# Kernel tuning notes

Hardware: AMD Instinct MI355X
Metric: run time of the kernel (lower is better)

Reference implementation:

```python
import jax, jax.numpy as jnp
import numpy as np

B, S, D = 32, 1024, 256
K, H, L = 64, 4, 4
KH, DV = K // H, D // H  # pooling key size per head, pooling value size
EPS = 1e-5
SCALE = 1.0 / np.sqrt(K).astype(np.float32)  # both encoder and pooling use sqrt(1/key_size)


def _ln(x, gamma=None, beta=None):
    m = jnp.mean(x, axis=-1, keepdims=True)
    v = jnp.mean(jnp.square(x - m), axis=-1, keepdims=True)
    y = (x - m) * jax.lax.rsqrt(v + EPS)
    if gamma is not None:
        y = y * gamma + beta
    return y


def setup_inputs() -> dict:
    key = jax.random.key(0)
    ks = iter(jax.random.split(key, 32))

    def w(shape, fan_in):
        return jax.random.normal(next(ks), shape, jnp.float32) / np.sqrt(fan_in).astype(np.float32)

    inp = {
        "input": jax.random.normal(next(ks), (B, S, D), jnp.float32),
        "lin0_W": w((D, D), D), "lin0_b": jnp.zeros((D,), jnp.float32),
        # stacked params for the 4 AttentionEncoder layers
        "enc_Wk": w((L, D, K), D), "enc_bk": jnp.zeros((L, K), jnp.float32),
        "enc_Wq": w((L, D, K), D), "enc_bq": jnp.zeros((L, K), jnp.float32),
        "enc_Wv": w((L, D, D), D), "enc_bv": jnp.zeros((L, D), jnp.float32),
        "enc_Wb": w((L, D, 1), D), "enc_bb": jnp.zeros((L, 1), jnp.float32),
        "enc_Wff": w((L, D, D), D), "enc_bff": jnp.zeros((L, D), jnp.float32),
        "enc_g1": jnp.ones((L, D), jnp.float32), "enc_beta1": jnp.zeros((L, D), jnp.float32),
        # multi-head pooling head
        "pool_Wk": w((D, KH), D), "pool_bk": jnp.zeros((KH,), jnp.float32),
        "pool_Wv": w((D, DV), D), "pool_bv": jnp.zeros((DV,), jnp.float32),
        "queries": jax.random.normal(next(ks), (H, KH), jnp.float32),
        "lin1_W": w((D, 2), D), "lin1_b": jnp.zeros((2,), jnp.float32),
    }
    return inp


def reference(input, lin0_W, lin0_b, enc_Wk, enc_bk, enc_Wq, enc_bq, enc_Wv, enc_bv,
              enc_Wb, enc_bb, enc_Wff, enc_bff, enc_g1, enc_beta1,
              pool_Wk, pool_bk, pool_Wv, pool_bv, queries, lin1_W, lin1_b):
    # NOTE: original code computes act0(lin0(input)) and then discards it (dead code);
    # it is omitted here since it does not affect the output.
    x = input
    for i in range(L):
        k = (x @ enc_Wk[i] + enc_bk[i]) * SCALE          # [B,S,K]
        q = x @ enc_Wq[i] + enc_bq[i]                     # [B,S,K]
        v = x @ enc_Wv[i] + enc_bv[i]                     # [B,S,D]
        bias = x @ enc_Wb[i] + enc_bb[i]                  # [B,S,1], broadcast over columns
        scores = jax.nn.sigmoid(jnp.einsum('bik,bjk->bij', k, q) + bias)  # [B,S,S]
        attn = jnp.einsum('bij,bjd->bid', scores, v)      # [B,S,D]
        res = _ln(x + attn, enc_g1[i], enc_beta1[i])
        ff = jax.nn.relu(res @ enc_Wff[i] + enc_bff[i])
        x = _ln(res + ff)                                 # norm2: no affine
    # multi-head pooling with learned queries
    pk = (x @ pool_Wk + pool_bk) * SCALE                  # [B,S,KH]
    pv = x @ pool_Wv + pool_bv                            # [B,S,DV]
    sc = jnp.einsum('bsk,hk->bsh', pk, queries)           # [B,S,H]
    sc = jax.nn.softmax(sc, axis=1)                       # softmax over sequence
    pooled = jnp.einsum('bsh,bsd->bhd', sc, pv).reshape(x.shape[0], -1)  # [B, H*DV]=[B,D]
    return pooled @ lin1_W + lin1_b                       # [B,2]
```

## Files before the change

kernel.cpp:

```cpp
#include <hip/hip_runtime.h>
#include <hip/hip_bf16.h>
#include <math.h>

#define BB 32
#define SS 1024
#define DD 256
#define MM (BB*SS)
#define LEPS 1e-5f

typedef __bf16 bf16x8 __attribute__((ext_vector_type(8)));
typedef __bf16 bf16x4 __attribute__((ext_vector_type(4)));
typedef float f32x4 __attribute__((ext_vector_type(4)));

__global__ __launch_bounds__(256) void cast_wt(const float* __restrict__ W,
                                               __bf16* __restrict__ WT,
                                               int N, float scale, int dstride, int noff) {
    int n = blockIdx.x, l = blockIdx.z, k = threadIdx.x;
    WT[(size_t)dstride * l + (size_t)(n + noff) * 256 + k] =
        (__bf16)(W[(size_t)256 * N * l + (size_t)k * N + n] * scale);
}

__global__ __launch_bounds__(128) void bias_combine(const float* __restrict__ bk,
                                                    const float* __restrict__ bq,
                                                    float* __restrict__ dst) {
    int l = blockIdx.x, j = threadIdx.x;
    dst[l * 128 + j] = (j < 64) ? bk[l * 64 + j] * 0.125f : bq[l * 64 + (j - 64)];
}

__global__ __launch_bounds__(256) void cast_x(const float* __restrict__ x, __bf16* __restrict__ xb) {
    size_t i = ((size_t)blockIdx.x * 256 + threadIdx.x) * 8;
    float4 a = *(const float4*)(x + i);
    float4 b = *(const float4*)(x + i + 4);
    __bf16 o[8] __attribute__((aligned(16)));
    o[0] = (__bf16)a.x; o[1] = (__bf16)a.y; o[2] = (__bf16)a.z; o[3] = (__bf16)a.w;
    o[4] = (__bf16)b.x; o[5] = (__bf16)b.y; o[6] = (__bf16)b.z; o[7] = (__bf16)b.w;
    *(bf16x8*)(xb + i) = *(bf16x8*)o;
}

template <int BN, int MODE>
__global__ __launch_bounds__(256) void gemm_mfma(const __bf16* __restrict__ A,
                                                 const __bf16* __restrict__ WT,
                                                 const float* __restrict__ bias,
                                                 float bscale, int relu,
                                                 void* __restrict__ Cv, void* __restrict__ Cv2,
                                                 int N) {
    constexpr int MR = (BN == 128) ? 4 : 2;
    constexpr int NC = (BN == 128) ? 4 : BN / 16;
    const int t = threadIdx.x;
    const int w = t >> 6, lane = t & 63;
    const int m0 = blockIdx.x * 128;
    const int n0 = blockIdx.y * BN;
    const size_t wt_z = (MODE == 3) ? (size_t)blockIdx.z * SS * 256 : 0;
    const size_t c_z  = (MODE == 3) ? (size_t)blockIdx.z * 256 * (size_t)N : 0;
    const int wr = (BN == 128) ? (w >> 1) * 64 : w * 32;
    const int wc = (BN == 128) ? (w & 1) * 64 : 0;
    __shared__ __align__(16) __bf16 Al[128][64];
    __shared__ __align__(16) __bf16 Wl[BN][64];
    f32x4 acc[MR][NC] = {};

    for (int k0 = 0; k0 < 256; k0 += 64) {
        __syncthreads();
        {
            int r = t >> 1, half = t & 1;
            const __bf16* src = A + (size_t)(m0 + r) * 256 + k0 + half * 32;
            bf16x8 v0 = *(const bf16x8*)(src);
            bf16x8 v1 = *(const bf16x8*)(src + 8);
            bf16x8 v2 = *(const bf16x8*)(src + 16);
            bf16x8 v3 = *(const bf16x8*)(src + 24);
            int cb = half * 4;
            *(bf16x8*)&Al[r][((cb + 0) ^ (r & 7)) * 8] = v0;
            *(bf16x8*)&Al[r][((cb + 1) ^ (r & 7)) * 8] = v1;
            *(bf16x8*)&Al[r][((cb + 2) ^ (r & 7)) * 8] = v2;
            *(bf16x8*)&Al[r][((cb + 3) ^ (r & 7)) * 8] = v3;
        }
        if (BN == 128) {
            int r = t >> 1, half = t & 1;
            const __bf16* src = WT + wt_z + (size_t)(n0 + r) * 256 + k0 + half * 32;
            bf16x8 v0 = *(const bf16x8*)(src);
            bf16x8 v1 = *(const bf16x8*)(src + 8);
            bf16x8 v2 = *(const bf16x8*)(src + 16);
            bf16x8 v3 = *(const bf16x8*)(src + 24);
            int cb = half * 4;
            *(bf16x8*)&Wl[r][((cb + 0) ^ (r & 7)) * 8] = v0;
            *(bf16x8*)&Wl[r][((cb + 1) ^ (r & 7)) * 8] = v1;
            *(bf16x8*)&Wl[r][((cb + 2) ^ (r & 7)) * 8] = v2;
            *(bf16x8*)&Wl[r][((cb + 3) ^ (r & 7)) * 8] = v3;
        } else if (BN == 64) {
            int n = t >> 2, q = t & 3;
            const __bf16* src = WT + (size_t)(n0 + n) * 256 + k0 + q * 16;
            bf16x8 v0 = *(const bf16x8*)src;
            bf16x8 v1 = *(const bf16x8*)(src + 8);
            *(bf16x8*)&Wl[n][((q * 2 + 0) ^ (n & 7)) * 8] = v0;
            *(bf16x8*)&Wl[n][((q * 2 + 1) ^ (n & 7)) * 8] = v1;
        } else {
            if (t < 128) {
                int n = t >> 3, c = t & 7;
                bf16x8 v = *(const bf16x8*)(WT + (size_t)(n0 + n) * 256 + k0 + c * 8);
                *(bf16x8*)&Wl[n][(c ^ (n & 7)) * 8] = v;
            }
        }
        __syncthreads();
#pragma unroll
        for (int ks = 0; ks < 2; ks++) {
            int c = ks * 4 + (lane >> 4);
            bf16x8 af[MR];
#pragma unroll
            for (int mf = 0; mf < MR; mf++) {
                int i = wr + mf * 16 + (lane & 15);
                af[mf] = *(const bf16x8*)&Al[i][(c ^ (i & 7)) * 8];
            }
#pragma unroll
            for (int nf = 0; nf < NC; nf++) {
                int n = wc + nf * 16 + (lane & 15);
                bf16x8 bfr = *(const bf16x8*)&Wl[n][(c ^ (n & 7)) * 8];
#pragma unroll
                for (int mf = 0; mf < MR; mf++)
                    acc[mf][nf] = __builtin_amdgcn_mfma_f32_16x16x32_bf16(af[mf], bfr, acc[mf][nf], 0, 0, 0);
            }
        }
    }
#pragma unroll
    for (int mf = 0; mf < MR; mf++) {
#pragma unroll
        for (int nf = 0; nf < NC; nf++) {
            int col = n0 + wc + nf * 16 + (lane & 15);
            float bcol = (MODE == 3) ? 0.f : bias[col] * bscale;
#pragma unroll
            for (int r = 0; r < 4; r++) {
                int row = m0 + wr + mf * 16 + (lane >> 4) * 4 + r;
                float v = acc[mf][nf][r] + ((MODE == 3) ? bias[row] : bcol);
                if (relu) v = fmaxf(v, 0.f);
                if (MODE == 2) {
                    if (col < 64) ((__bf16*)Cv)[(size_t)row * 64 + col] = (__bf16)v;
                    else ((__bf16*)Cv2)[(size_t)row * 64 + (col - 64)] = (__bf16)v;
                } else if (MODE == 1 || MODE == 3) {
                    ((__bf16*)Cv)[c_z + (size_t)row * N + col] = (__bf16)v;
                } else {
                    ((float*)Cv)[(size_t)row * N + col] = v;
                }
            }
        }
    }
}

__global__ __launch_bounds__(256) void bias_gemv(const float* __restrict__ X,
                                                 const float* __restrict__ Wb,
                                                 const float* __restrict__ bb,
                                                 float* __restrict__ out) {
    int wave = threadIdx.x >> 6, lane = threadIdx.x & 63;
    size_t row = (size_t)blockIdx.x * 4 + wave;
    float4 xv = *(const float4*)(X + row * 256 + lane * 4);
    float4 wv = *(const float4*)(Wb + lane * 4);
    float p = xv.x * wv.x + xv.y * wv.y + xv.z * wv.z + xv.w * wv.w;
    for (int off = 32; off; off >>= 1) p += __shfl_down(p, off, 64);
    if (lane == 0) out[row] = p + bb[0];
}

__global__ __launch_bounds__(512, 4) void attn_mfma(const __bf16* __restrict__ kb,
                                                    const __bf16* __restrict__ qb,
                                                    const __bf16* __restrict__ vT,
                                                    const float* __restrict__ biasb,
                                                    const float* __restrict__ xin,
                                                    const float* __restrict__ gamma,
                                                    const float* __restrict__ beta,
                                                    float* __restrict__ outf,
                                                    __bf16* __restrict__ outb) {
    int h = blockIdx.x;
    int blow = h & 7, rest = h >> 3;
    int ib = rest & 15;
    int b = blow + (rest >> 4) * 8;
    const int i0 = ib * 64;
    const int t = threadIdx.x;
    const int w = t >> 6, lane = t & 63;
    const int iq = w >> 1;
    const int dhalf = w & 1;

    __shared__ __align__(16) __bf16 Kl[64][64];
    __shared__ __align__(16) __bf16 Ql[64][64];
    __shared__ __align__(16) __bf16 Vl[256][64];
    __shared__ __align__(16) __bf16 Sl[64][64];
    __shared__ float bsh[64];
    __shared__ float rowred[2][64][2];

    {
        int i = t >> 3, c = t & 7;
        bf16x8 v = *(const bf16x8*)(kb + ((size_t)(b * SS + i0 + i)) * 64 + c * 8);
        *(bf16x8*)&Kl[i][(c ^ (i & 7)) * 8] = v;
        if (t < 64) bsh[t] = biasb[b * SS + i0 + t];
    }

    f32x4 acc[8] = {};

    for (int j0 = 0; j0 < SS; j0 += 64) {
        __syncthreads();
        {
            int j = t >> 3, c = t & 7;
            bf16x8 v = *(const bf16x8*)(qb + ((size_t)(b * SS + j0 + j)) * 64 + c * 8);
            *(bf16x8*)&Ql[j][(c ^ (j & 7)) * 8] = v;
        }
        {
            int d = t >> 1, jh = t & 1;
            const __bf16* src = vT + ((size_t)b * 256 + d) * SS + j0 + jh * 32;
#pragma unroll
            for (int u = 0; u < 4; u++) {
                bf16x8 v = *(const bf16x8*)(src + u * 8);
                *(bf16x8*)&Vl[d][((jh * 4 + u) ^ (d & 7)) * 8] = v;
            }
        }
        __syncthreads();
#pragma unroll
        for (int jj = 0; jj < 2; jj++) {
            int jq = (w & 1) * 2 + jj;
            f32x4 sacc = {0.f, 0.f, 0.f, 0.f};
#pragma unroll
            for (int ks = 0; ks < 2; ks++) {
                int i = iq * 16 + (lane & 15);
                int ck = ks * 4 + (lane >> 4);
                bf16x8 a = *(const bf16x8*)&Kl[i][(ck ^ (i & 7)) * 8];
                int j = jq * 16 + (lane & 15);
                bf16x8 bq = *(const bf16x8*)&Ql[j][(ck ^ (j & 7)) * 8];
                sacc = __builtin_amdgcn_mfma_f32_16x16x32_bf16(a, bq, sacc, 0, 0, 0);
            }
            int jcol = jq * 16 + (lane & 15);
#pragma unroll
            for (int r = 0; r < 4; r++) {
                int irow = iq * 16 + (lane >> 4) * 4 + r;
                float x = sacc[r] + bsh[irow];
                float sg = 1.f / (1.f + __expf(-x));
                Sl[irow][(((jcol >> 3) ^ (irow & 7)) * 8) + (jcol & 7)] = (__bf16)sg;
            }
        }
        __syncthreads();
        bf16x8 am[2];
#pragma unroll
        for (int m = 0; m < 2; m++) {
            int i = iq * 16 + (lane & 15);
            int cj = m * 4 + (lane >> 4);
            am[m] = *(const bf16x8*)&Sl[i][(cj ^ (i & 7)) * 8];
        }
#pragma unroll
        for (int dq = 0; dq < 8; dq++) {
            int d = dhalf * 128 + dq * 16 + (lane & 15);
#pragma unroll
            for (int m = 0; m < 2; m++) {
                int cj = m * 4 + (lane >> 4);
                bf16x8 bv = *(const bf16x8*)&Vl[d][(cj ^ (d & 7)) * 8];
                acc[dq] = __builtin_amdgcn_mfma_f32_16x16x32_bf16(am[m], bv, acc[dq], 0, 0, 0);
            }
        }
    }

#pragma unroll
    for (int r = 0; r < 4; r++) {
        int il = iq * 16 + (lane >> 4) * 4 + r;
        size_t rowoff = ((size_t)(b * SS + i0 + il)) * 256 + dhalf * 128 + (lane & 15);
#pragma unroll
        for (int dq = 0; dq < 8; dq++)
            acc[dq][r] += xin[rowoff + dq * 16];
    }
    float sr[4], qr[4];
#pragma unroll
    for (int r = 0; r < 4; r++) {
        float s = 0.f, q = 0.f;
#pragma unroll
        for (int dq = 0; dq < 8; dq++) {
            float v = acc[dq][r];
            s += v; q += v * v;
        }
#pragma unroll
        for (int mask = 8; mask; mask >>= 1) {
            s += __shfl_xor(s, mask, 64);
            q += __shfl_xor(q, mask, 64);
        }
        sr[r] = s; qr[r] = q;
    }
    if ((lane & 15) == 0) {
#pragma unroll
        for (int r = 0; r < 4; r++) {
            int il = iq * 16 + (lane >> 4) * 4 + r;
            rowred[dhalf][il][0] = sr[r];
            rowred[dhalf][il][1] = qr[r];
        }
    }
    __syncthreads();
    float gv[8], bv2[8];
#pragma unroll
    for (int dq = 0; dq < 8; dq++) {
        int d = dhalf * 128 + dq * 16 + (lane & 15);
        gv[dq] = gamma[d];
        bv2[dq] = beta[d];
    }
#pragma unroll
    for (int r = 0; r < 4; r++) {
        int il = iq * 16 + (lane >> 4) * 4 + r;
        float st = rowred[0][il][0] + rowred[1][il][0];
        float qt = rowred[0][il][1] + rowred[1][il][1];
        float mean = st * (1.f / 256.f);
        float var = qt * (1.f / 256.f) - mean * mean;
        float inv = 1.f / sqrtf(var + LEPS);
        size_t rowoff = ((size_t)(b * SS + i0 + il)) * 256 + dhalf * 128 + (lane & 15);
#pragma unroll
        for (int dq = 0; dq < 8; dq++) {
            float o = (acc[dq][r] - mean) * inv * gv[dq] + bv2[dq];
            outf[rowoff + dq * 16] = o;
            outb[rowoff + dq * 16] = (__bf16)o;
        }
    }
}

__global__ __launch_bounds__(512) void gemm_ff_ln2(const __bf16* __restrict__ A,
                                                   const __bf16* __restrict__ WT,
                                                   const float* __restrict__ bias,
                                                   const float* __restrict__ resid,
                                                   float* __restrict__ outf,
                                                   __bf16* __restrict__ outb) {
    const int t = threadIdx.x;
    const int w = t >> 6, lane = t & 63;
    const int m0 = blockIdx.x * 128;
    const int wr = (w >> 2) * 64, wc = (w & 3) * 64;
    __shared__ __align__(16) __bf16 Al[128][64];
    __shared__ __align__(16) __bf16 Wl[256][64];
    __shared__ float rowred[4][128][2];
    f32x4 acc[4][4] = {};

    for (int k0 = 0; k0 < 256; k0 += 64) {
        __syncthreads();
        {
            int r = t >> 2, c0 = (t & 3) * 2;
            const __bf16* src = A + (size_t)(m0 + r) * 256 + k0 + c0 * 8;
            bf16x8 v0 = *(const bf16x8*)src;
            bf16x8 v1 = *(const bf16x8*)(src + 8);
            *(bf16x8*)&Al[r][((c0 + 0) ^ (r & 7)) * 8] = v0;
            *(bf16x8*)&Al[r][((c0 + 1) ^ (r & 7)) * 8] = v1;
        }
        {
            int n = t >> 1, c0 = (t & 1) * 4;
            const __bf16* src = WT + (size_t)n * 256 + k0 + c0 * 8;
#pragma unroll
            for (int u = 0; u < 4; u++) {
                bf16x8 v = *(const bf16x8*)(src + u * 8);
                *(bf16x8*)&Wl[n][((c0 + u) ^ (n & 7)) * 8] = v;
            }
        }
        __syncthreads();
#pragma unroll
        for (int ks = 0; ks < 2; ks++) {
            int c = ks * 4 + (lane >> 4);
            bf16x8 af[4];
#pragma unroll
            for (int mf = 0; mf < 4; mf++) {
                int i = wr + mf * 16 + (lane & 15);
                af[mf] = *(const bf16x8*)&Al[i][(c ^ (i & 7)) * 8];
            }
#pragma unroll
            for (int nf = 0; nf < 4; nf++) {
                int n = wc + nf * 16 + (lane & 15);
                bf16x8 bfr = *(const bf16x8*)&Wl[n][(c ^ (n & 7)) * 8];
#pragma unroll
                for (int mf = 0; mf < 4; mf++)
                    acc[mf][nf] = __builtin_amdgcn_mfma_f32_16x16x32_bf16(af[mf], bfr, acc[mf][nf], 0, 0, 0);
            }
        }
    }
    float colb[4];
#pragma unroll
    for (int nf = 0; nf < 4; nf++) colb[nf] = bias[wc + nf * 16 + (lane & 15)];
#pragma unroll
    for (int mf = 0; mf < 4; mf++) {
#pragma unroll
        for (int r = 0; r < 4; r++) {
            int rl = wr + mf * 16 + (lane >> 4) * 4 + r;
            const float* rrow = resid + (size_t)(m0 + rl) * 256 + wc + (lane & 15);
            float s = 0.f, q = 0.f;
#pragma unroll
            for (int nf = 0; nf < 4; nf++) {
                float v = fmaxf(acc[mf][nf][r] + colb[nf], 0.f) + rrow[nf * 16];
                acc[mf][nf][r] = v;
                s += v; q += v * v;
            }
#pragma unroll
            for (int msk = 1; msk <= 8; msk <<= 1) {
                s += __shfl_xor(s, msk, 64);
                q += __shfl_xor(q, msk, 64);
            }
            if ((lane & 15) == 0) {
                rowred[w & 3][rl][0] = s;
                rowred[w & 3][rl][1] = q;
            }
        }
    }
    __syncthreads();
#pragma unroll
    for (int mf = 0; mf < 4; mf++) {
#pragma unroll
        for (int r = 0; r < 4; r++) {
            int rl = wr + mf * 16 + (lane >> 4) * 4 + r;
            float s = rowred[0][rl][0] + rowred[1][rl][0] + rowred[2][rl][0] + rowred[3][rl][0];
            float q = rowred[0][rl][1] + rowred[1][rl][1] + rowred[2][rl][1] + rowred[3][rl][1];
            float mean = s * (1.f / 256.f);
            float var = q * (1.f / 256.f) - mean * mean;
            float inv = 1.f / sqrtf(var + LEPS);
            size_t base = (size_t)(m0 + rl) * 256 + wc + (lane & 15);
#pragma unroll
            for (int nf = 0; nf < 4; nf++) {
                float o = (acc[mf][nf][r] - mean) * inv;
                outf[base + nf * 16] = o;
                outb[base + nf * 16] = (__bf16)o;
            }
        }
    }
}

__global__ __launch_bounds__(256) void pool_kernel(const float* __restrict__ pk,
                                                   const float* __restrict__ pv,
                                                   const float* __restrict__ queries,
                                                   const float* __restrict__ W1,
                                                   const float* __restrict__ b1,
                                                   float* __restrict__ out) {
    const int b = blockIdx.x;
    const int t = threadIdx.x;
    __shared__ float sc[4][1024];
    __shared__ float qv[4][16];
    __shared__ float redsum[4];
    __shared__ float r0[256], r1[256];
    if (t < 64) qv[t >> 4][t & 15] = queries[t];
    __syncthreads();
    for (int c = 0; c < 4; c++) {
        int s = c * 256 + t;
        const float* p = pk + ((size_t)b * SS + s) * 16;
        float4 a0 = *(const float4*)p;
        float4 a1 = *(const float4*)(p + 4);
        float4 a2 = *(const float4*)(p + 8);
        float4 a3 = *(const float4*)(p + 12);
#pragma unroll
        for (int hh = 0; hh < 4; hh++) {
            float d = a0.x * qv[hh][0] + a0.y * qv[hh][1] + a0.z * qv[hh][2] + a0.w * qv[hh][3]
                    + a1.x * qv[hh][4] + a1.y * qv[hh][5] + a1.z * qv[hh][6] + a1.w * qv[hh][7]
                    + a2.x * qv[hh][8] + a2.y * qv[hh][9] + a2.z * qv[hh][10] + a2.w * qv[hh][11]
                    + a3.x * qv[hh][12] + a3.y * qv[hh][13] + a3.z * qv[hh][14] + a3.w * qv[hh][15];
            sc[hh][s] = d;
        }
    }
    __syncthreads();
    {
        int hh = t >> 6, lane = t & 63;
        float m = -1e30f;
        for (int s = lane; s < 1024; s += 64) m = fmaxf(m, sc[hh][s]);
        for (int off = 32; off; off >>= 1) m = fmaxf(m, __shfl_down(m, off, 64));
        m = __shfl(m, 0, 64);
        float sum = 0.f;
        for (int s = lane; s < 1024; s += 64) {
            float e = expf(sc[hh][s] - m);
            sc[hh][s] = e;
            sum += e;
        }
        for (int off = 32; off; off >>= 1) sum += __shfl_down(sum, off, 64);
        if (lane == 0) redsum[hh] = sum;
    }
    __syncthreads();
    int hh = t >> 6, d = t & 63;
    float acc = 0.f;
    for (int s = 0; s < 1024; s++) acc += sc[hh][s] * pv[((size_t)b * SS + s) * 64 + d];
    acc /= redsum[hh];
    float p0 = acc * W1[t * 2 + 0];
    float p1 = acc * W1[t * 2 + 1];
    r0[t] = p0; r1[t] = p1;
    __syncthreads();
    for (int off = 128; off > 0; off >>= 1) {
        if (t < off) { r0[t] += r0[t + off]; r1[t] += r1[t + off]; }
        __syncthreads();
    }
    if (t == 0) {
        out[b * 2 + 0] = r0[0] + b1[0];
        out[b * 2 + 1] = r1[0] + b1[1];
    }
}

extern "C" void kernel_launch(void* const* d_in, const int* in_sizes, int n_in,
                              void* d_out, int out_size, void* d_ws, size_t ws_size,
                              hipStream_t stream) {
    const float* input = (const float*)d_in[0];
    const float* eWk = (const float*)d_in[3];
    const float* ebk = (const float*)d_in[4];
    const float* eWq = (const float*)d_in[5];
    const float* ebq = (const float*)d_in[6];
    const float* eWv = (const float*)d_in[7];
    const float* ebv = (const float*)d_in[8];
    const float* eWb = (const float*)d_in[9];
    const float* ebb = (const float*)d_in[10];
    const float* eWff = (const float*)d_in[11];
    const float* ebff = (const float*)d_in[12];
    const float* eg1 = (const float*)d_in[13];
    const float* ebe1 = (const float*)d_in[14];
    const float* pWk = (const float*)d_in[15];
    const float* pbk = (const float*)d_in[16];
    const float* pWv = (const float*)d_in[17];
    const float* pbv = (const float*)d_in[18];
    const float* qrs = (const float*)d_in[19];
    const float* W1 = (const float*)d_in[20];
    const float* b1 = (const float*)d_in[21];
    float* out = (float*)d_out;

    float* ws = (float*)d_ws;
    float* xbuf = ws;
    __bf16* xbf = (__bf16*)(xbuf + (size_t)MM * DD);
    float* tmp2 = (float*)(xbf + (size_t)MM * DD);
    float* r3 = tmp2 + (size_t)MM * DD;
    __bf16* tmp2bf = (__bf16*)r3;
    __bf16* vTb = tmp2bf + (size_t)MM * DD;
    float* r4 = r3 + (size_t)MM * DD;
    __bf16* kbf = (__bf16*)r4;
    __bf16* qbf = kbf + (size_t)MM * 64;
    float* bbuf = r4 + (size_t)MM * (DD / 2);
    __bf16* wbf = (__bf16*)(bbuf + MM);

    __bf16* WkqT = wbf;
    __bf16* WvT = WkqT + 4 * 128 * 256;
    __bf16* WffT = WvT + 4 * 256 * 256;
    __bf16* pWkT = WffT + 4 * 256 * 256;
    __bf16* pWvT = pWkT + 16 * 256;
    float* biasc = (float*)(pWvT + 64 * 256);

    float* pkbuf = tmp2;
    float* pvbuf = tmp2 + (size_t)MM * 16;

    const float SC = 0.125f;

    cast_wt<<<dim3(64, 1, 4), 256, 0, stream>>>(eWk, WkqT, 64, SC, 128 * 256, 0);
    cast_wt<<<dim3(64, 1, 4), 256, 0, stream>>>(eWq, WkqT, 64, 1.f, 128 * 256, 64);
    cast_wt<<<dim3(256, 1, 4), 256, 0, stream>>>(eWv, WvT, 256, 1.f, 256 * 256, 0);
    cast_wt<<<dim3(256, 1, 4), 256, 0, stream>>>(eWff, WffT, 256, 1.f, 256 * 256, 0);
    cast_wt<<<dim3(16, 1, 1), 256, 0, stream>>>(pWk, pWkT, 16, SC, 16 * 256, 0);
    cast_wt<<<dim3(64, 1, 1), 256, 0, stream>>>(pWv, pWvT, 64, 1.f, 64 * 256, 0);
    bias_combine<<<4, 128, 0, stream>>>(ebk, ebq, biasc);
    cast_x<<<MM * DD / (256 * 8), 256, 0, stream>>>(input, xbf);

    for (int l = 0; l < 4; l++) {
        const float* xin = (l == 0) ? input : xbuf;
        gemm_mfma<128, 2><<<dim3(MM / 128, 1), 256, 0, stream>>>(
            xbf, WkqT + (size_t)l * 128 * 256, biasc + l * 128, 1.f, 0, kbf, qbf, 64);
        gemm_mfma<128, 3><<<dim3(2, SS / 128, BB), 256, 0, stream>>>(
            WvT + (size_t)l * 256 * 256, xbf, ebv + l * DD, 1.f, 0, vTb, nullptr, SS);
        bias_gemv<<<MM / 4, 256, 0, stream>>>(xin, eWb + (size_t)l * DD, ebb + l, bbuf);
        attn_mfma<<<dim3(512, 1), 512, 0, stream>>>(kbf, qbf, vTb, bbuf, xin,
                                                    eg1 + l * DD, ebe1 + l * DD, tmp2, tmp2bf);
        gemm_ff_ln2<<<dim3(MM / 128, 1), 512, 0, stream>>>(
            tmp2bf, WffT + (size_t)l * 256 * 256, ebff + l * DD, tmp2, xbuf, xbf);
    }
    gemm_mfma<16, 0><<<dim3(MM / 128, 1), 256, 0, stream>>>(xbf, pWkT, pbk, SC, 0, pkbuf, nullptr, 16);
    gemm_mfma<64, 0><<<dim3(MM / 128, 1), 256, 0, stream>>>(xbf, pWvT, pbv, 1.f, 0, pvbuf, nullptr, 64);
    pool_kernel<<<BB, 256, 0, stream>>>(pkbuf, pvbuf, qrs, W1, b1, out);
}
```

Baseline: 491.1 us.

## Prefetch next Q/V tiles into registers during attention compute, add setprio

The attention kernel now issues global loads for the next Q and V tile into registers before computing the current tile, then writes them to LDS after a barrier. This hides global load latency behind the MFMA work. MFMA sections are wrapped in s_setprio to favour issuing matrix ops. Separately, bias_gemv now reads the bf16 copy of x instead of fp32, which halves its traffic at a small precision cost. The prefetch raises register pressure under launch_bounds(512,4).

```diff
diff --git a/kernel.cpp b/kernel.cpp
--- a/kernel.cpp
+++ b/kernel.cpp
@@ -143,15 +143,15 @@
     }
 }
 
-__global__ __launch_bounds__(256) void bias_gemv(const float* __restrict__ X,
+__global__ __launch_bounds__(256) void bias_gemv(const __bf16* __restrict__ X,
                                                  const float* __restrict__ Wb,
                                                  const float* __restrict__ bb,
                                                  float* __restrict__ out) {
     int wave = threadIdx.x >> 6, lane = threadIdx.x & 63;
     size_t row = (size_t)blockIdx.x * 4 + wave;
-    float4 xv = *(const float4*)(X + row * 256 + lane * 4);
+    bf16x4 xv = *(const bf16x4*)(X + row * 256 + lane * 4);
     float4 wv = *(const float4*)(Wb + lane * 4);
-    float p = xv.x * wv.x + xv.y * wv.y + xv.z * wv.z + xv.w * wv.w;
+    float p = (float)xv[0] * wv.x + (float)xv[1] * wv.y + (float)xv[2] * wv.z + (float)xv[3] * wv.w;
     for (int off = 32; off; off >>= 1) p += __shfl_down(p, off, 64);
     if (lane == 0) out[row] = p + bb[0];
 }
@@ -182,36 +182,47 @@
     __shared__ float bsh[64];
     __shared__ float rowred[2][64][2];
 
+    const int qj = t >> 3, qc = t & 7;
+    const __bf16* qsrc_base = qb + ((size_t)(b * SS + qj)) * 64 + qc * 8;
+    const int vd = t >> 1, vjh = t & 1;
+    const __bf16* vsrc_base = vT + ((size_t)b * 256 + vd) * SS + vjh * 32;
+
     {
         int i = t >> 3, c = t & 7;
         bf16x8 v = *(const bf16x8*)(kb + ((size_t)(b * SS + i0 + i)) * 64 + c * 8);
         *(bf16x8*)&Kl[i][(c ^ (i & 7)) * 8] = v;
         if (t < 64) bsh[t] = biasb[b * SS + i0 + t];
     }
+    {
+        bf16x8 qv = *(const bf16x8*)(qsrc_base);
+        *(bf16x8*)&Ql[qj][(qc ^ (qj & 7)) * 8] = qv;
+#pragma unroll
+        for (int u = 0; u < 4; u++) {
+            bf16x8 v = *(const bf16x8*)(vsrc_base + u * 8);
+            *(bf16x8*)&Vl[vd][((vjh * 4 + u) ^ (vd & 7)) * 8] = v;
+        }
+    }
+    __syncthreads();
 
     f32x4 acc[8] = {};
 
     for (int j0 = 0; j0 < SS; j0 += 64) {
-        __syncthreads();
-        {
-            int j = t >> 3, c = t & 7;
-            bf16x8 v = *(const bf16x8*)(qb + ((size_t)(b * SS + j0 + j)) * 64 + c * 8);
-            *(bf16x8*)&Ql[j][(c ^ (j & 7)) * 8] = v;
-        }
-        {
-            int d = t >> 1, jh = t & 1;
-            const __bf16* src = vT + ((size_t)b * 256 + d) * SS + j0 + jh * 32;
-#pragma unroll
-            for (int u = 0; u < 4; u++) {
-                bf16x8 v = *(const bf16x8*)(src + u * 8);
-                *(bf16x8*)&Vl[d][((jh * 4 + u) ^ (d & 7)) * 8] = v;
-            }
-        }
-        __syncthreads();
+        const bool has_next = (j0 + 64) < SS;
+        bf16x8 qn;
+        bf16x8 vn0, vn1, vn2, vn3;
+        if (has_next) {
+            qn = *(const bf16x8*)(qsrc_base + (size_t)(j0 + 64) * 64);
+            const __bf16* vs = vsrc_base + j0 + 64;
+            vn0 = *(const bf16x8*)(vs);
+            vn1 = *(const bf16x8*)(vs + 8);
+            vn2 = *(const bf16x8*)(vs + 16);
+            vn3 = *(const bf16x8*)(vs + 24);
+        }
 #pragma unroll
         for (int jj = 0; jj < 2; jj++) {
             int jq = (w & 1) * 2 + jj;
             f32x4 sacc = {0.f, 0.f, 0.f, 0.f};
+            __builtin_amdgcn_s_setprio(1);
 #pragma unroll
             for (int ks = 0; ks < 2; ks++) {
                 int i = iq * 16 + (lane & 15);
@@ -221,6 +232,7 @@
                 bf16x8 bq = *(const bf16x8*)&Ql[j][(ck ^ (j & 7)) * 8];
                 sacc = __builtin_amdgcn_mfma_f32_16x16x32_bf16(a, bq, sacc, 0, 0, 0);
             }
+            __builtin_amdgcn_s_setprio(0);
             int jcol = jq * 16 + (lane & 15);
 #pragma unroll
             for (int r = 0; r < 4; r++) {
@@ -238,6 +250,7 @@
             int cj = m * 4 + (lane >> 4);
             am[m] = *(const bf16x8*)&Sl[i][(cj ^ (i & 7)) * 8];
         }
+        __builtin_amdgcn_s_setprio(1);
 #pragma unroll
         for (int dq = 0; dq < 8; dq++) {
             int d = dhalf * 128 + dq * 16 + (lane & 15);
@@ -247,6 +260,16 @@
                 bf16x8 bv = *(const bf16x8*)&Vl[d][(cj ^ (d & 7)) * 8];
                 acc[dq] = __builtin_amdgcn_mfma_f32_16x16x32_bf16(am[m], bv, acc[dq], 0, 0, 0);
             }
+        }
+        __builtin_amdgcn_s_setprio(0);
+        __syncthreads();
+        if (has_next) {
+            *(bf16x8*)&Ql[qj][(qc ^ (qj & 7)) * 8] = qn;
+            *(bf16x8*)&Vl[vd][((vjh * 4 + 0) ^ (vd & 7)) * 8] = vn0;
+            *(bf16x8*)&Vl[vd][((vjh * 4 + 1) ^ (vd & 7)) * 8] = vn1;
+            *(bf16x8*)&Vl[vd][((vjh * 4 + 2) ^ (vd & 7)) * 8] = vn2;
+            *(bf16x8*)&Vl[vd][((vjh * 4 + 3) ^ (vd & 7)) * 8] = vn3;
+            __syncthreads();
         }
     }
 
@@ -541,7 +564,7 @@
             xbf, WkqT + (size_t)l * 128 * 256, biasc + l * 128, 1.f, 0, kbf, qbf, 64);
         gemm_mfma<128, 3><<<dim3(2, SS / 128, BB), 256, 0, stream>>>(
             WvT + (size_t)l * 256 * 256, xbf, ebv + l * DD, 1.f, 0, vTb, nullptr, SS);
-        bias_gemv<<<MM / 4, 256, 0, stream>>>(xin, eWb + (size_t)l * DD, ebb + l, bbuf);
+        bias_gemv<<<MM / 4, 256, 0, stream>>>(xbf, eWb + (size_t)l * DD, ebb + l, bbuf);
         attn_mfma<<<dim3(512, 1), 512, 0, stream>>>(kbf, qbf, vTb, bbuf, xin,
                                                     eg1 + l * DD, ebe1 + l * DD, tmp2, tmp2bf);
         gemm_ff_ln2<<<dim3(MM / 128, 1), 512, 0, stream>>>(
```

Result: no change. 485.7 us (-1.1%).
